# Kernel optimization log

Measured on AMD Instinct MI355X. Metric: run time of the kernel, lower is better.

The kernel has to match this reference:

```python
import jax, jax.numpy as jnp
import numpy as np

IOTA = 1.0 / 137.0
PHI = 0.618033988749894
N_SAMPLE = 5
N_SYM = 2048
HIDDEN = 2048
N_LIN_IN = 3
N_LIN_OUT = 9
EPS = 1e-9


def _instance_norm(x):
    # InstanceNorm1d, affine=False, unbatched (C, L): per-row mean/biased-var over last dim
    m = jnp.mean(x, axis=-1, keepdims=True)
    v = jnp.mean((x - m) ** 2, axis=-1, keepdims=True)
    return (x - m) * jax.lax.rsqrt(v + EPS)


def _lstm_cell(x, W_ih, W_hh, b_ih, b_hh):
    # torch.nn.LSTMCell with h0 = c0 = 0: the W_hh recurrent term is identically zero,
    # and f*c0 vanishes. Gate order (torch): i, f, g, o.
    gates = x @ W_ih.T + b_ih + b_hh  # [B, 4*HIDDEN]
    i, f, g, o = jnp.split(gates, 4, axis=-1)
    c = jax.nn.sigmoid(i) * jnp.tanh(g)
    return jax.nn.sigmoid(o) * jnp.tanh(c)


def setup_inputs() -> dict:
    key = jax.random.key(0)
    ks = jax.random.split(key, 10)
    s = 0.02
    return dict(
        signal=jax.random.normal(ks[0], (N_SAMPLE, N_SYM), jnp.float32),
        u1=jax.random.uniform(ks[1], (N_LIN_OUT, N_SYM), jnp.float32),
        u2=jax.random.uniform(ks[2], (N_LIN_OUT, HIDDEN), jnp.float32),
        bil_W=jax.random.normal(ks[3], (N_LIN_OUT, N_LIN_IN, N_LIN_IN), jnp.float32) * s,
        bil_b=jnp.zeros((N_LIN_OUT,), jnp.float32),
        Wih1=jax.random.normal(ks[4], (4 * HIDDEN, N_SYM), jnp.float32) * s,
        Whh1=jax.random.normal(ks[5], (4 * HIDDEN, HIDDEN), jnp.float32) * s,
        bih1=jnp.zeros((4 * HIDDEN,), jnp.float32),
        bhh1=jnp.zeros((4 * HIDDEN,), jnp.float32),
        Wih2=jax.random.normal(ks[6], (4 * HIDDEN, HIDDEN), jnp.float32) * s,
        Whh2=jax.random.normal(ks[7], (4 * HIDDEN, HIDDEN), jnp.float32) * s,
        bih2=jnp.zeros((4 * HIDDEN,), jnp.float32),
        bhh2=jnp.zeros((4 * HIDDEN,), jnp.float32),
        lin_W=jax.random.normal(ks[8], (N_SAMPLE * N_SYM, HIDDEN), jnp.float32) * s,
        lin_b=jnp.zeros((N_SAMPLE * N_SYM,), jnp.float32),
    )


def reference(signal, u1, u2, bil_W, bil_b, Wih1, Whh1, bih1, bhh1,
              Wih2, Whh2, bih2, bhh2, lin_W, lin_b):
    x = _instance_norm(signal.T)                    # [N_SYM, 5]
    fr = jnp.fft.rfft(x, axis=-1)                   # [N_SYM, 3] complex64
    b = jnp.nan_to_num(fr.real * fr.imag, nan=IOTA, posinf=1.0, neginf=IOTA)
    b = jax.nn.softmax(jax.nn.sigmoid(b), axis=1)   # [N_SYM, 3]
    # nn.Bilinear: out[n,k] = x1[n,i] W[k,i,j] x2[n,j] + b[k]
    b = jnp.einsum('ni,kij,nj->nk', b, bil_W, b) + bil_b  # [N_SYM, 9]
    b = IOTA + b.T * (u1 < PHI).astype(b.dtype)     # stochastic mask -> [9, N_SYM]
    h = _lstm_cell(b, Wih1, Whh1, bih1, bhh1)       # [9, HIDDEN]
    h = IOTA + h * (u2 < PHI).astype(h.dtype)
    h = _lstm_cell(h, Wih2, Whh2, bih2, bhh2)       # [9, HIDDEN]
    out = (h @ lin_W.T + lin_b).reshape(N_SAMPLE, N_SYM, N_LIN_OUT)  # view([5, N_SYM, 9])
    out = jax.nn.softmax(_instance_norm(out.sum(2)), axis=1)         # [5, N_SYM]
    return out
```

## Files before the change

### kernel.cpp

```cpp
#include <hip/hip_runtime.h>
#include <math.h>

#define IOTA_F (1.0f / 137.0f)
#define PHI_F  0.618033988749894f

__device__ __forceinline__ float sigm(float x) { return 1.0f / (1.0f + expf(-x)); }

__device__ __forceinline__ float nan2num(float v) {
    if (isnan(v)) return IOTA_F;
    if (isinf(v)) return v > 0.0f ? 1.0f : IOTA_F;
    return v;
}

__global__ void k_pre(const float* __restrict__ signal,
                      const float* __restrict__ u1,
                      const float* __restrict__ bilW,
                      const float* __restrict__ bilb,
                      float* __restrict__ B1)
{
    int s = blockIdx.x * blockDim.x + threadIdx.x;
    if (s >= 2048) return;

    float x0 = signal[0 * 2048 + s];
    float x1 = signal[1 * 2048 + s];
    float x2 = signal[2 * 2048 + s];
    float x3 = signal[3 * 2048 + s];
    float x4 = signal[4 * 2048 + s];

    float mean = (x0 + x1 + x2 + x3 + x4) * 0.2f;
    float d0 = x0 - mean, d1 = x1 - mean, d2 = x2 - mean, d3 = x3 - mean, d4 = x4 - mean;
    float var = (d0 * d0 + d1 * d1 + d2 * d2 + d3 * d3 + d4 * d4) * 0.2f;
    float r = 1.0f / sqrtf(var + 1e-9f);
    d0 *= r; d1 *= r; d2 *= r; d3 *= r; d4 *= r;

    const float c1 = 0.30901699437494742f;
    const float c2 = -0.80901699437494745f;
    const float s1 = 0.95105651629515357f;
    const float s2 = 0.58778525229247314f;

    float re1 = d0 + c1 * (d1 + d4) + c2 * (d2 + d3);
    float im1 = -(s1 * (d1 - d4) + s2 * (d2 - d3));
    float re2 = d0 + c2 * (d1 + d4) + c1 * (d2 + d3);
    float im2 = -s2 * (d1 - d4) + s1 * (d2 - d3);

    float p1 = nan2num(re1 * im1);
    float p2 = nan2num(re2 * im2);
    float g0 = 0.5f;
    float g1 = sigm(p1);
    float g2 = sigm(p2);

    float mx = fmaxf(g0, fmaxf(g1, g2));
    float e0 = expf(g0 - mx), e1 = expf(g1 - mx), e2 = expf(g2 - mx);
    float inv = 1.0f / (e0 + e1 + e2);
    float w[3] = { e0 * inv, e1 * inv, e2 * inv };

    #pragma unroll
    for (int kk = 0; kk < 9; ++kk) {
        float acc = bilb[kk];
        #pragma unroll
        for (int i = 0; i < 3; ++i)
            #pragma unroll
            for (int j = 0; j < 3; ++j)
                acc += w[i] * bilW[kk * 9 + i * 3 + j] * w[j];
        float mask = (u1[kk * 2048 + s] < PHI_F) ? 1.0f : 0.0f;
        B1[kk * 2048 + s] = IOTA_F + acc * mask;
    }
}

template <bool MASK>
__global__ __launch_bounds__(256) void k_lstm_fused(
    const float* __restrict__ Bv,
    const float* __restrict__ W,
    const float* __restrict__ b1,
    const float* __restrict__ b2,
    const float* __restrict__ u,
    float* __restrict__ Bout)
{
    __shared__ float lds[4][4][3][9];

    const int tid  = threadIdx.x;
    const int w    = tid >> 6;
    const int lane = tid & 63;
    const int grp  = lane >> 4;
    const int li   = lane & 15;

    const int q = blockIdx.x * 4 + grp;

    const float4* __restrict__ B4 = reinterpret_cast<const float4*>(Bv);
    const float4* __restrict__ Wi = reinterpret_cast<const float4*>(W) + (size_t)q * 512;
    const float4* __restrict__ Wg = Wi + (size_t)4096 * 512;
    const float4* __restrict__ Wo = Wi + (size_t)6144 * 512;

    float acc[3][9];
    #pragma unroll
    for (int r = 0; r < 3; ++r)
        #pragma unroll
        for (int m = 0; m < 9; ++m) acc[r][m] = 0.0f;

    const int kb4 = w * 128;

    #pragma unroll 2
    for (int it = 0; it < 8; ++it) {
        const int idx = kb4 + it * 16 + li;
        float4 bv[9];
        #pragma unroll
        for (int m = 0; m < 9; ++m) bv[m] = B4[m * 512 + idx];
        float4 wv0 = Wi[idx];
        float4 wv1 = Wg[idx];
        float4 wv2 = Wo[idx];
        #pragma unroll
        for (int m = 0; m < 9; ++m) {
            acc[0][m] = fmaf(wv0.x, bv[m].x, acc[0][m]);
            acc[0][m] = fmaf(wv0.y, bv[m].y, acc[0][m]);
            acc[0][m] = fmaf(wv0.z, bv[m].z, acc[0][m]);
            acc[0][m] = fmaf(wv0.w, bv[m].w, acc[0][m]);
            acc[1][m] = fmaf(wv1.x, bv[m].x, acc[1][m]);
            acc[1][m] = fmaf(wv1.y, bv[m].y, acc[1][m]);
            acc[1][m] = fmaf(wv1.z, bv[m].z, acc[1][m]);
            acc[1][m] = fmaf(wv1.w, bv[m].w, acc[1][m]);
            acc[2][m] = fmaf(wv2.x, bv[m].x, acc[2][m]);
            acc[2][m] = fmaf(wv2.y, bv[m].y, acc[2][m]);
            acc[2][m] = fmaf(wv2.z, bv[m].z, acc[2][m]);
            acc[2][m] = fmaf(wv2.w, bv[m].w, acc[2][m]);
        }
    }

    #pragma unroll
    for (int r = 0; r < 3; ++r)
        #pragma unroll
        for (int m = 0; m < 9; ++m) {
            float v = acc[r][m];
            v += __shfl_xor(v, 1);
            v += __shfl_xor(v, 2);
            v += __shfl_xor(v, 4);
            v += __shfl_xor(v, 8);
            acc[r][m] = v;
        }

    if (li == 0) {
        #pragma unroll
        for (int r = 0; r < 3; ++r)
            #pragma unroll
            for (int m = 0; m < 9; ++m)
                lds[w][grp][r][m] = acc[r][m];
    }
    __syncthreads();

    if (tid < 36) {
        const int qq = tid / 9;
        const int m  = tid - qq * 9;
        const int qg = blockIdx.x * 4 + qq;
        float iv = lds[0][qq][0][m] + lds[1][qq][0][m] + lds[2][qq][0][m] + lds[3][qq][0][m];
        float gv = lds[0][qq][1][m] + lds[1][qq][1][m] + lds[2][qq][1][m] + lds[3][qq][1][m];
        float ov = lds[0][qq][2][m] + lds[1][qq][2][m] + lds[2][qq][2][m] + lds[3][qq][2][m];
        iv += b1[qg] + b2[qg];
        gv += b1[4096 + qg] + b2[4096 + qg];
        ov += b1[6144 + qg] + b2[6144 + qg];
        float c = sigm(iv) * tanhf(gv);
        float h = sigm(ov) * tanhf(c);
        if (MASK) h = IOTA_F + h * ((u[m * 2048 + qg] < PHI_F) ? 1.0f : 0.0f);
        Bout[m * 2048 + qg] = h;
    }
}

template <int R>
__global__ __launch_bounds__(256) void k_gemvR(
    const float* __restrict__ Bv,
    const float* __restrict__ W,
    const float* __restrict__ bias,
    float* __restrict__ Out,
    int nrows)
{
    __shared__ float lds[4][4 * R][9];

    const int tid  = threadIdx.x;
    const int w    = tid >> 6;
    const int lane = tid & 63;
    const int grp  = lane >> 4;
    const int li   = lane & 15;

    const int rowB = blockIdx.x * 4 * R;
    const int row0 = rowB + grp * R;

    const float4* __restrict__ B4 = reinterpret_cast<const float4*>(Bv);
    const float4* __restrict__ W0 = reinterpret_cast<const float4*>(W) + (size_t)row0 * 512;

    float acc[R][9];
    #pragma unroll
    for (int r = 0; r < R; ++r)
        #pragma unroll
        for (int m = 0; m < 9; ++m) acc[r][m] = 0.0f;

    const int kb4 = w * 128;

    #pragma unroll 2
    for (int it = 0; it < 8; ++it) {
        const int idx = kb4 + it * 16 + li;
        float4 bv[9];
        #pragma unroll
        for (int m = 0; m < 9; ++m) bv[m] = B4[m * 512 + idx];
        #pragma unroll
        for (int r = 0; r < R; ++r) {
            float4 wv = W0[(size_t)r * 512 + idx];
            #pragma unroll
            for (int m = 0; m < 9; ++m) {
                acc[r][m] = fmaf(wv.x, bv[m].x, acc[r][m]);
                acc[r][m] = fmaf(wv.y, bv[m].y, acc[r][m]);
                acc[r][m] = fmaf(wv.z, bv[m].z, acc[r][m]);
                acc[r][m] = fmaf(wv.w, bv[m].w, acc[r][m]);
            }
        }
    }

    #pragma unroll
    for (int r = 0; r < R; ++r)
        #pragma unroll
        for (int m = 0; m < 9; ++m) {
            float v = acc[r][m];
            v += __shfl_xor(v, 1);
            v += __shfl_xor(v, 2);
            v += __shfl_xor(v, 4);
            v += __shfl_xor(v, 8);
            acc[r][m] = v;
        }

    if (li == 0) {
        #pragma unroll
        for (int r = 0; r < R; ++r)
            #pragma unroll
            for (int m = 0; m < 9; ++m)
                lds[w][grp * R + r][m] = acc[r][m];
    }
    __syncthreads();

    for (int t = tid; t < 4 * R * 9; t += 256) {
        const int row = t / 9;
        const int m   = t - row * 9;
        float v = lds[0][row][m] + lds[1][row][m] + lds[2][row][m] + lds[3][row][m];
        const int grow = rowB + row;
        Out[(size_t)m * nrows + grow] = v + bias[grow];
    }
}

__device__ __forceinline__ float block_reduce(float v, float* red, int tid, int op) {
    #pragma unroll
    for (int off = 32; off > 0; off >>= 1) {
        float o = __shfl_xor(v, off);
        v = op ? fmaxf(v, o) : (v + o);
    }
    __syncthreads();
    if ((tid & 63) == 0) red[tid >> 6] = v;
    __syncthreads();
    float r = red[0];
    #pragma unroll
    for (int w = 1; w < 8; ++w) r = op ? fmaxf(r, red[w]) : (r + red[w]);
    return r;
}

__global__ void k_final(const float* __restrict__ Z,
                        float* __restrict__ out)
{
    __shared__ float t[2048];
    __shared__ float red[8];
    const int a = blockIdx.x;
    const int tid = threadIdx.x;

    for (int s = tid; s < 2048; s += 512) {
        const float* zp = Z + a * 18432 + s * 9;
        float acc = 0.0f;
        #pragma unroll
        for (int k = 0; k < 9; ++k) acc += zp[k];
        t[s] = acc;
    }
    __syncthreads();

    float l0 = t[tid], l1 = t[tid + 512], l2 = t[tid + 1024], l3 = t[tid + 1536];

    float ssum = block_reduce(l0 + l1 + l2 + l3, red, tid, 0);
    float mean = ssum * (1.0f / 2048.0f);
    float e0 = l0 - mean, e1 = l1 - mean, e2 = l2 - mean, e3 = l3 - mean;
    float vsum = block_reduce(e0 * e0 + e1 * e1 + e2 * e2 + e3 * e3, red, tid, 0);
    float rstd = 1.0f / sqrtf(vsum * (1.0f / 2048.0f) + 1e-9f);
    float xn0 = e0 * rstd, xn1 = e1 * rstd, xn2 = e2 * rstd, xn3 = e3 * rstd;

    float mx = block_reduce(fmaxf(fmaxf(xn0, xn1), fmaxf(xn2, xn3)), red, tid, 1);
    float ex0 = expf(xn0 - mx), ex1 = expf(xn1 - mx), ex2 = expf(xn2 - mx), ex3 = expf(xn3 - mx);
    float esum = block_reduce(ex0 + ex1 + ex2 + ex3, red, tid, 0);
    float inv = 1.0f / esum;

    out[a * 2048 + tid]        = ex0 * inv;
    out[a * 2048 + tid + 512]  = ex1 * inv;
    out[a * 2048 + tid + 1024] = ex2 * inv;
    out[a * 2048 + tid + 1536] = ex3 * inv;
}

extern "C" void kernel_launch(void* const* d_in, const int* in_sizes, int n_in,
                              void* d_out, int out_size, void* d_ws, size_t ws_size,
                              hipStream_t stream)
{
    const float* signal = (const float*)d_in[0];
    const float* u1     = (const float*)d_in[1];
    const float* u2     = (const float*)d_in[2];
    const float* bilW   = (const float*)d_in[3];
    const float* bilb   = (const float*)d_in[4];
    const float* Wih1   = (const float*)d_in[5];
    const float* bih1   = (const float*)d_in[7];
    const float* bhh1   = (const float*)d_in[8];
    const float* Wih2   = (const float*)d_in[9];
    const float* bih2   = (const float*)d_in[11];
    const float* bhh2   = (const float*)d_in[12];
    const float* linW   = (const float*)d_in[13];
    const float* linb   = (const float*)d_in[14];

    float* out = (float*)d_out;
    float* ws  = (float*)d_ws;

    float* B1 = ws;
    float* B2 = ws + 18432;
    float* B3 = B1;
    float* Z  = ws + 36864;

    k_pre<<<8, 256, 0, stream>>>(signal, u1, bilW, bilb, B1);

    k_lstm_fused<true><<<512, 256, 0, stream>>>(B1, Wih1, bih1, bhh1, u2, B2);
    k_lstm_fused<false><<<512, 256, 0, stream>>>(B2, Wih2, bih2, bhh2, nullptr, B3);

    k_gemvR<5><<<512, 256, 0, stream>>>(B3, linW, linb, Z, 10240);

    k_final<<<5, 512, 0, stream>>>(Z, out);
}
```

Baseline: 56.06 us.

## Split K across 8 groups per row and prefetch weights into registers

The LSTM and final GEMV kernels now split the 2048-long reduction into 8 chunks spread over the sixteen 16-lane groups of each block. Each block handles 2 rows instead of 4, which doubles the grid to 1024 blocks. All weight float4s for a thread are loaded up front so more bytes are in flight per thread, and activations are loaded one m at a time. The aim is more memory-level parallelism and occupancy for these bandwidth-bound weight streams, at the cost of a wider cross-group LDS reduction and more blocks. The preprocessing kernel's launch shape changes from 8x256 to 32x64.

```diff
diff --git a/kernel.cpp b/kernel.cpp
--- a/kernel.cpp
+++ b/kernel.cpp
@@ -76,7 +76,7 @@
     const float* __restrict__ u,
     float* __restrict__ Bout)
 {
-    __shared__ float lds[4][4][3][9];
+    __shared__ float lds[2][8][3][9];
 
     const int tid  = threadIdx.x;
     const int w    = tid >> 6;
@@ -84,12 +84,24 @@
     const int grp  = lane >> 4;
     const int li   = lane & 15;
 
-    const int q = blockIdx.x * 4 + grp;
+    const int G  = w * 4 + grp;
+    const int qi = G >> 3;
+    const int kc = G & 7;
+    const int q  = blockIdx.x * 2 + qi;
 
     const float4* __restrict__ B4 = reinterpret_cast<const float4*>(Bv);
     const float4* __restrict__ Wi = reinterpret_cast<const float4*>(W) + (size_t)q * 512;
-    const float4* __restrict__ Wg = Wi + (size_t)4096 * 512;
-    const float4* __restrict__ Wo = Wi + (size_t)6144 * 512;
+
+    const int kb4 = kc * 64;
+
+    float4 wp[3][4];
+    #pragma unroll
+    for (int it = 0; it < 4; ++it) {
+        const int idx = kb4 + it * 16 + li;
+        wp[0][it] = Wi[idx];
+        wp[1][it] = Wi[(size_t)4096 * 512 + idx];
+        wp[2][it] = Wi[(size_t)6144 * 512 + idx];
+    }
 
     float acc[3][9];
     #pragma unroll
@@ -97,31 +109,19 @@
         #pragma unroll
         for (int m = 0; m < 9; ++m) acc[r][m] = 0.0f;
 
-    const int kb4 = w * 128;
-
-    #pragma unroll 2
-    for (int it = 0; it < 8; ++it) {
+    #pragma unroll
+    for (int it = 0; it < 4; ++it) {
         const int idx = kb4 + it * 16 + li;
-        float4 bv[9];
-        #pragma unroll
-        for (int m = 0; m < 9; ++m) bv[m] = B4[m * 512 + idx];
-        float4 wv0 = Wi[idx];
-        float4 wv1 = Wg[idx];
-        float4 wv2 = Wo[idx];
         #pragma unroll
         for (int m = 0; m < 9; ++m) {
-            acc[0][m] = fmaf(wv0.x, bv[m].x, acc[0][m]);
-            acc[0][m] = fmaf(wv0.y, bv[m].y, acc[0][m]);
-            acc[0][m] = fmaf(wv0.z, bv[m].z, acc[0][m]);
-            acc[0][m] = fmaf(wv0.w, bv[m].w, acc[0][m]);
-            acc[1][m] = fmaf(wv1.x, bv[m].x, acc[1][m]);
-            acc[1][m] = fmaf(wv1.y, bv[m].y, acc[1][m]);
-            acc[1][m] = fmaf(wv1.z, bv[m].z, acc[1][m]);
-            acc[1][m] = fmaf(wv1.w, bv[m].w, acc[1][m]);
-            acc[2][m] = fmaf(wv2.x, bv[m].x, acc[2][m]);
-            acc[2][m] = fmaf(wv2.y, bv[m].y, acc[2][m]);
-            acc[2][m] = fmaf(wv2.z, bv[m].z, acc[2][m]);
-            acc[2][m] = fmaf(wv2.w, bv[m].w, acc[2][m]);
+            float4 bv = B4[m * 512 + idx];
+            #pragma unroll
+            for (int r = 0; r < 3; ++r) {
+                acc[r][m] = fmaf(wp[r][it].x, bv.x, acc[r][m]);
+                acc[r][m] = fmaf(wp[r][it].y, bv.y, acc[r][m]);
+                acc[r][m] = fmaf(wp[r][it].z, bv.z, acc[r][m]);
+                acc[r][m] = fmaf(wp[r][it].w, bv.w, acc[r][m]);
+            }
         }
     }
 
@@ -142,17 +142,21 @@
         for (int r = 0; r < 3; ++r)
             #pragma unroll
             for (int m = 0; m < 9; ++m)
-                lds[w][grp][r][m] = acc[r][m];
-    }
-    __syncthreads();
-
-    if (tid < 36) {
+                lds[qi][kc][r][m] = acc[r][m];
+    }
+    __syncthreads();
+
+    if (tid < 18) {
         const int qq = tid / 9;
         const int m  = tid - qq * 9;
-        const int qg = blockIdx.x * 4 + qq;
-        float iv = lds[0][qq][0][m] + lds[1][qq][0][m] + lds[2][qq][0][m] + lds[3][qq][0][m];
-        float gv = lds[0][qq][1][m] + lds[1][qq][1][m] + lds[2][qq][1][m] + lds[3][qq][1][m];
-        float ov = lds[0][qq][2][m] + lds[1][qq][2][m] + lds[2][qq][2][m] + lds[3][qq][2][m];
+        const int qg = blockIdx.x * 2 + qq;
+        float iv = 0.0f, gv = 0.0f, ov = 0.0f;
+        #pragma unroll
+        for (int k = 0; k < 8; ++k) {
+            iv += lds[qq][k][0][m];
+            gv += lds[qq][k][1][m];
+            ov += lds[qq][k][2][m];
+        }
         iv += b1[qg] + b2[qg];
         gv += b1[4096 + qg] + b2[4096 + qg];
         ov += b1[6144 + qg] + b2[6144 + qg];
@@ -171,7 +175,7 @@
     float* __restrict__ Out,
     int nrows)
 {
-    __shared__ float lds[4][4 * R][9];
+    __shared__ float lds[2][8][R][9];
 
     const int tid  = threadIdx.x;
     const int w    = tid >> 6;
@@ -179,35 +183,47 @@
     const int grp  = lane >> 4;
     const int li   = lane & 15;
 
-    const int rowB = blockIdx.x * 4 * R;
-    const int row0 = rowB + grp * R;
+    const int G  = w * 4 + grp;
+    const int h  = G >> 3;
+    const int kc = G & 7;
+
+    const int rowB = blockIdx.x * 2 * R;
+    const int row0 = rowB + h * R;
 
     const float4* __restrict__ B4 = reinterpret_cast<const float4*>(Bv);
     const float4* __restrict__ W0 = reinterpret_cast<const float4*>(W) + (size_t)row0 * 512;
 
+    const int kb4 = kc * 64;
+
     float acc[R][9];
     #pragma unroll
     for (int r = 0; r < R; ++r)
         #pragma unroll
         for (int m = 0; m < 9; ++m) acc[r][m] = 0.0f;
 
-    const int kb4 = w * 128;
-
-    #pragma unroll 2
-    for (int it = 0; it < 8; ++it) {
-        const int idx = kb4 + it * 16 + li;
-        float4 bv[9];
-        #pragma unroll
-        for (int m = 0; m < 9; ++m) bv[m] = B4[m * 512 + idx];
-        #pragma unroll
-        for (int r = 0; r < R; ++r) {
-            float4 wv = W0[(size_t)r * 512 + idx];
+    #pragma unroll
+    for (int st = 0; st < 2; ++st) {
+        float4 wp[R][2];
+        #pragma unroll
+        for (int it = 0; it < 2; ++it) {
+            const int idx = kb4 + (st * 2 + it) * 16 + li;
+            #pragma unroll
+            for (int r = 0; r < R; ++r)
+                wp[r][it] = W0[(size_t)r * 512 + idx];
+        }
+        #pragma unroll
+        for (int it = 0; it < 2; ++it) {
+            const int idx = kb4 + (st * 2 + it) * 16 + li;
             #pragma unroll
             for (int m = 0; m < 9; ++m) {
-                acc[r][m] = fmaf(wv.x, bv[m].x, acc[r][m]);
-                acc[r][m] = fmaf(wv.y, bv[m].y, acc[r][m]);
-                acc[r][m] = fmaf(wv.z, bv[m].z, acc[r][m]);
-                acc[r][m] = fmaf(wv.w, bv[m].w, acc[r][m]);
+                float4 bv = B4[m * 512 + idx];
+                #pragma unroll
+                for (int r = 0; r < R; ++r) {
+                    acc[r][m] = fmaf(wp[r][it].x, bv.x, acc[r][m]);
+                    acc[r][m] = fmaf(wp[r][it].y, bv.y, acc[r][m]);
+                    acc[r][m] = fmaf(wp[r][it].z, bv.z, acc[r][m]);
+                    acc[r][m] = fmaf(wp[r][it].w, bv.w, acc[r][m]);
+                }
             }
         }
     }
@@ -229,14 +245,18 @@
         for (int r = 0; r < R; ++r)
             #pragma unroll
             for (int m = 0; m < 9; ++m)
-                lds[w][grp * R + r][m] = acc[r][m];
-    }
-    __syncthreads();
-
-    for (int t = tid; t < 4 * R * 9; t += 256) {
-        const int row = t / 9;
-        const int m   = t - row * 9;
-        float v = lds[0][row][m] + lds[1][row][m] + lds[2][row][m] + lds[3][row][m];
+                lds[h][kc][r][m] = acc[r][m];
+    }
+    __syncthreads();
+
+    if (tid < 2 * R * 9) {
+        const int row = tid / 9;
+        const int m   = tid - row * 9;
+        const int hh  = row / R;
+        const int rr  = row - hh * R;
+        float v = 0.0f;
+        #pragma unroll
+        for (int k = 0; k < 8; ++k) v += lds[hh][k][rr][m];
         const int grow = rowB + row;
         Out[(size_t)m * nrows + grow] = v + bias[grow];
     }
@@ -320,12 +340,12 @@
     float* B3 = B1;
     float* Z  = ws + 36864;
 
-    k_pre<<<8, 256, 0, stream>>>(signal, u1, bilW, bilb, B1);
-
-    k_lstm_fused<true><<<512, 256, 0, stream>>>(B1, Wih1, bih1, bhh1, u2, B2);
-    k_lstm_fused<false><<<512, 256, 0, stream>>>(B2, Wih2, bih2, bhh2, nullptr, B3);
-
-    k_gemvR<5><<<512, 256, 0, stream>>>(B3, linW, linb, Z, 10240);
+    k_pre<<<32, 64, 0, stream>>>(signal, u1, bilW, bilb, B1);
+
+    k_lstm_fused<true><<<1024, 256, 0, stream>>>(B1, Wih1, bih1, bhh1, u2, B2);
+    k_lstm_fused<false><<<1024, 256, 0, stream>>>(B2, Wih2, bih2, bhh2, nullptr, B3);
+
+    k_gemvR<5><<<1024, 256, 0, stream>>>(B3, linW, linb, Z, 10240);
 
     k_final<<<5, 512, 0, stream>>>(Z, out);
 }
```

Measured after the change: 61.95 us. 1.1x slower.

## Fuse preprocessing into first LSTM kernel and final softmax into last GEMV

Applied to the files above, without the earlier changes.

Each block of the first LSTM kernel now recomputes the full normalization/FFT/bilinear preprocessing into shared memory, removing the separate pre kernel. The final instance-norm/softmax is folded into the output GEMV using an atomic counter so the last finishing block performs it. This removes two kernel launches and a global round trip, at the cost of redundant per-block preprocessing work, large LDS usage limiting occupancy, and a serialized single-block tail.

```diff
diff --git a/kernel.cpp b/kernel.cpp
--- a/kernel.cpp
+++ b/kernel.cpp
@@ -3,6 +3,7 @@
 
 #define IOTA_F (1.0f / 137.0f)
 #define PHI_F  0.618033988749894f
+#define NBLK   512
 
 __device__ __forceinline__ float sigm(float x) { return 1.0f / (1.0f + expf(-x)); }
 
@@ -12,68 +13,167 @@
     return v;
 }
 
-__global__ void k_pre(const float* __restrict__ signal,
-                      const float* __restrict__ u1,
-                      const float* __restrict__ bilW,
-                      const float* __restrict__ bilb,
-                      float* __restrict__ B1)
-{
-    int s = blockIdx.x * blockDim.x + threadIdx.x;
-    if (s >= 2048) return;
-
-    float x0 = signal[0 * 2048 + s];
-    float x1 = signal[1 * 2048 + s];
-    float x2 = signal[2 * 2048 + s];
-    float x3 = signal[3 * 2048 + s];
-    float x4 = signal[4 * 2048 + s];
-
-    float mean = (x0 + x1 + x2 + x3 + x4) * 0.2f;
-    float d0 = x0 - mean, d1 = x1 - mean, d2 = x2 - mean, d3 = x3 - mean, d4 = x4 - mean;
-    float var = (d0 * d0 + d1 * d1 + d2 * d2 + d3 * d3 + d4 * d4) * 0.2f;
-    float r = 1.0f / sqrtf(var + 1e-9f);
-    d0 *= r; d1 *= r; d2 *= r; d3 *= r; d4 *= r;
-
-    const float c1 = 0.30901699437494742f;
-    const float c2 = -0.80901699437494745f;
-    const float s1 = 0.95105651629515357f;
-    const float s2 = 0.58778525229247314f;
-
-    float re1 = d0 + c1 * (d1 + d4) + c2 * (d2 + d3);
-    float im1 = -(s1 * (d1 - d4) + s2 * (d2 - d3));
-    float re2 = d0 + c2 * (d1 + d4) + c1 * (d2 + d3);
-    float im2 = -s2 * (d1 - d4) + s1 * (d2 - d3);
-
-    float p1 = nan2num(re1 * im1);
-    float p2 = nan2num(re2 * im2);
-    float g0 = 0.5f;
-    float g1 = sigm(p1);
-    float g2 = sigm(p2);
-
-    float mx = fmaxf(g0, fmaxf(g1, g2));
-    float e0 = expf(g0 - mx), e1 = expf(g1 - mx), e2 = expf(g2 - mx);
-    float inv = 1.0f / (e0 + e1 + e2);
-    float w[3] = { e0 * inv, e1 * inv, e2 * inv };
-
-    #pragma unroll
-    for (int kk = 0; kk < 9; ++kk) {
-        float acc = bilb[kk];
-        #pragma unroll
-        for (int i = 0; i < 3; ++i)
+__device__ void pre_into_lds(int tid,
+                             const float* __restrict__ signal,
+                             const float* __restrict__ u1,
+                             const float* __restrict__ bilW,
+                             const float* __restrict__ bilb,
+                             float* __restrict__ Bsf)
+{
+    #pragma unroll
+    for (int k = 0; k < 8; ++k) {
+        const int s = k * 256 + tid;
+
+        float x0 = signal[0 * 2048 + s];
+        float x1 = signal[1 * 2048 + s];
+        float x2 = signal[2 * 2048 + s];
+        float x3 = signal[3 * 2048 + s];
+        float x4 = signal[4 * 2048 + s];
+
+        float mean = (x0 + x1 + x2 + x3 + x4) * 0.2f;
+        float d0 = x0 - mean, d1 = x1 - mean, d2 = x2 - mean, d3 = x3 - mean, d4 = x4 - mean;
+        float var = (d0 * d0 + d1 * d1 + d2 * d2 + d3 * d3 + d4 * d4) * 0.2f;
+        float r = 1.0f / sqrtf(var + 1e-9f);
+        d0 *= r; d1 *= r; d2 *= r; d3 *= r; d4 *= r;
+
+        const float c1 = 0.30901699437494742f;
+        const float c2 = -0.80901699437494745f;
+        const float s1 = 0.95105651629515357f;
+        const float s2 = 0.58778525229247314f;
+
+        float re1 = d0 + c1 * (d1 + d4) + c2 * (d2 + d3);
+        float im1 = -(s1 * (d1 - d4) + s2 * (d2 - d3));
+        float re2 = d0 + c2 * (d1 + d4) + c1 * (d2 + d3);
+        float im2 = -s2 * (d1 - d4) + s1 * (d2 - d3);
+
+        float p1 = nan2num(re1 * im1);
+        float p2 = nan2num(re2 * im2);
+        float g0 = 0.5f;
+        float g1 = sigm(p1);
+        float g2 = sigm(p2);
+
+        float mx = fmaxf(g0, fmaxf(g1, g2));
+        float e0 = expf(g0 - mx), e1 = expf(g1 - mx), e2 = expf(g2 - mx);
+        float inv = 1.0f / (e0 + e1 + e2);
+        float w[3] = { e0 * inv, e1 * inv, e2 * inv };
+
+        #pragma unroll
+        for (int kk = 0; kk < 9; ++kk) {
+            float acc = bilb[kk];
             #pragma unroll
-            for (int j = 0; j < 3; ++j)
-                acc += w[i] * bilW[kk * 9 + i * 3 + j] * w[j];
-        float mask = (u1[kk * 2048 + s] < PHI_F) ? 1.0f : 0.0f;
-        B1[kk * 2048 + s] = IOTA_F + acc * mask;
-    }
-}
-
-template <bool MASK>
-__global__ __launch_bounds__(256) void k_lstm_fused(
+            for (int i = 0; i < 3; ++i)
+                #pragma unroll
+                for (int j = 0; j < 3; ++j)
+                    acc += w[i] * bilW[kk * 9 + i * 3 + j] * w[j];
+            float mask = (u1[kk * 2048 + s] < PHI_F) ? 1.0f : 0.0f;
+            Bsf[kk * 2048 + s] = IOTA_F + acc * mask;
+        }
+    }
+}
+
+__global__ __launch_bounds__(256, 2) void k_pre_lstm1(
+    const float* __restrict__ signal, const float* __restrict__ u1,
+    const float* __restrict__ bilW, const float* __restrict__ bilb,
+    const float* __restrict__ W,
+    const float* __restrict__ b1,
+    const float* __restrict__ b2,
+    const float* __restrict__ u,
+    float* __restrict__ Bout)
+{
+    __shared__ float Bsf[9 * 2048];
+    __shared__ float red[4][4][3][9];
+
+    const int tid  = threadIdx.x;
+    const int w    = tid >> 6;
+    const int lane = tid & 63;
+    const int grp  = lane >> 4;
+    const int li   = lane & 15;
+
+    pre_into_lds(tid, signal, u1, bilW, bilb, Bsf);
+    __syncthreads();
+
+    const float4* __restrict__ Bs4 = reinterpret_cast<const float4*>(Bsf);
+    const int q = blockIdx.x * 4 + grp;
+
+    const float4* __restrict__ Wi = reinterpret_cast<const float4*>(W) + (size_t)q * 512;
+    const float4* __restrict__ Wg = Wi + (size_t)4096 * 512;
+    const float4* __restrict__ Wo = Wi + (size_t)6144 * 512;
+
+    float acc[3][9];
+    #pragma unroll
+    for (int r = 0; r < 3; ++r)
+        #pragma unroll
+        for (int m = 0; m < 9; ++m) acc[r][m] = 0.0f;
+
+    const int kb4 = w * 128;
+
+    #pragma unroll 2
+    for (int it = 0; it < 8; ++it) {
+        const int idx = kb4 + it * 16 + li;
+        float4 wv0 = Wi[idx];
+        float4 wv1 = Wg[idx];
+        float4 wv2 = Wo[idx];
+        #pragma unroll
+        for (int m = 0; m < 9; ++m) {
+            float4 bv = Bs4[m * 512 + idx];
+            acc[0][m] = fmaf(wv0.x, bv.x, acc[0][m]);
+            acc[0][m] = fmaf(wv0.y, bv.y, acc[0][m]);
+            acc[0][m] = fmaf(wv0.z, bv.z, acc[0][m]);
+            acc[0][m] = fmaf(wv0.w, bv.w, acc[0][m]);
+            acc[1][m] = fmaf(wv1.x, bv.x, acc[1][m]);
+            acc[1][m] = fmaf(wv1.y, bv.y, acc[1][m]);
+            acc[1][m] = fmaf(wv1.z, bv.z, acc[1][m]);
+            acc[1][m] = fmaf(wv1.w, bv.w, acc[1][m]);
+            acc[2][m] = fmaf(wv2.x, bv.x, acc[2][m]);
+            acc[2][m] = fmaf(wv2.y, bv.y, acc[2][m]);
+            acc[2][m] = fmaf(wv2.z, bv.z, acc[2][m]);
+            acc[2][m] = fmaf(wv2.w, bv.w, acc[2][m]);
+        }
+    }
+
+    #pragma unroll
+    for (int r = 0; r < 3; ++r)
+        #pragma unroll
+        for (int m = 0; m < 9; ++m) {
+            float v = acc[r][m];
+            v += __shfl_xor(v, 1);
+            v += __shfl_xor(v, 2);
+            v += __shfl_xor(v, 4);
+            v += __shfl_xor(v, 8);
+            acc[r][m] = v;
+        }
+
+    if (li == 0) {
+        #pragma unroll
+        for (int r = 0; r < 3; ++r)
+            #pragma unroll
+            for (int m = 0; m < 9; ++m)
+                red[w][grp][r][m] = acc[r][m];
+    }
+    __syncthreads();
+
+    if (tid < 36) {
+        const int qq = tid / 9;
+        const int m  = tid - qq * 9;
+        const int qg = blockIdx.x * 4 + qq;
+        float iv = red[0][qq][0][m] + red[1][qq][0][m] + red[2][qq][0][m] + red[3][qq][0][m];
+        float gv = red[0][qq][1][m] + red[1][qq][1][m] + red[2][qq][1][m] + red[3][qq][1][m];
+        float ov = red[0][qq][2][m] + red[1][qq][2][m] + red[2][qq][2][m] + red[3][qq][2][m];
+        iv += b1[qg] + b2[qg];
+        gv += b1[4096 + qg] + b2[4096 + qg];
+        ov += b1[6144 + qg] + b2[6144 + qg];
+        float c = sigm(iv) * tanhf(gv);
+        float h = sigm(ov) * tanhf(c);
+        h = IOTA_F + h * ((u[m * 2048 + qg] < PHI_F) ? 1.0f : 0.0f);
+        Bout[m * 2048 + qg] = h;
+    }
+}
+
+__global__ __launch_bounds__(256, 2) void k_lstm2(
     const float* __restrict__ Bv,
     const float* __restrict__ W,
     const float* __restrict__ b1,
     const float* __restrict__ b2,
-    const float* __restrict__ u,
     float* __restrict__ Bout)
 {
     __shared__ float lds[4][4][3][9];
@@ -158,20 +258,79 @@
         ov += b1[6144 + qg] + b2[6144 + qg];
         float c = sigm(iv) * tanhf(gv);
         float h = sigm(ov) * tanhf(c);
-        if (MASK) h = IOTA_F + h * ((u[m * 2048 + qg] < PHI_F) ? 1.0f : 0.0f);
         Bout[m * 2048 + qg] = h;
     }
 }
 
+__device__ __forceinline__ float block_reduce256(float v, float* red, int tid, int op) {
+    #pragma unroll
+    for (int off = 32; off > 0; off >>= 1) {
+        float o = __shfl_xor(v, off);
+        v = op ? fmaxf(v, o) : (v + o);
+    }
+    __syncthreads();
+    if ((tid & 63) == 0) red[tid >> 6] = v;
+    __syncthreads();
+    float r = op ? fmaxf(fmaxf(red[0], red[1]), fmaxf(red[2], red[3]))
+                 : (red[0] + red[1] + red[2] + red[3]);
+    return r;
+}
+
+__device__ void final_phase(int a, int tid, float* __restrict__ t, float* __restrict__ red,
+                            const float* __restrict__ Z, float* __restrict__ out)
+{
+    for (int s = tid; s < 2048; s += 256) {
+        const float* zp = Z + a * 18432 + s * 9;
+        float acc = 0.0f;
+        #pragma unroll
+        for (int k = 0; k < 9; ++k) acc += zp[k];
+        t[s] = acc;
+    }
+    __syncthreads();
+
+    float l[8];
+    #pragma unroll
+    for (int j = 0; j < 8; ++j) l[j] = t[tid + j * 256];
+
+    float lsum = 0.0f;
+    #pragma unroll
+    for (int j = 0; j < 8; ++j) lsum += l[j];
+    float ssum = block_reduce256(lsum, red, tid, 0);
+    float mean = ssum * (1.0f / 2048.0f);
+
+    float vs = 0.0f;
+    #pragma unroll
+    for (int j = 0; j < 8; ++j) { l[j] -= mean; vs += l[j] * l[j]; }
+    float vsum = block_reduce256(vs, red, tid, 0);
+    float rstd = 1.0f / sqrtf(vsum * (1.0f / 2048.0f) + 1e-9f);
+
+    float lmx = -1e30f;
+    #pragma unroll
+    for (int j = 0; j < 8; ++j) { l[j] *= rstd; lmx = fmaxf(lmx, l[j]); }
+    float mx = block_reduce256(lmx, red, tid, 1);
+
+    float es = 0.0f;
+    #pragma unroll
+    for (int j = 0; j < 8; ++j) { l[j] = expf(l[j] - mx); es += l[j]; }
+    float esum = block_reduce256(es, red, tid, 0);
+    float inv = 1.0f / esum;
+
+    #pragma unroll
+    for (int j = 0; j < 8; ++j)
+        out[a * 2048 + tid + j * 256] = l[j] * inv;
+}
+
 template <int R>
-__global__ __launch_bounds__(256) void k_gemvR(
+__global__ __launch_bounds__(256, 2) void k_gemvR_final(
     const float* __restrict__ Bv,
     const float* __restrict__ W,
     const float* __restrict__ bias,
-    float* __restrict__ Out,
-    int nrows)
-{
-    __shared__ float lds[4][4 * R][9];
+    float* __restrict__ Z,
+    float* __restrict__ out,
+    int* __restrict__ counter)
+{
+    __shared__ float arena[2052];
+    __shared__ int   is_last;
 
     const int tid  = threadIdx.x;
     const int w    = tid >> 6;
@@ -229,69 +388,35 @@
         for (int r = 0; r < R; ++r)
             #pragma unroll
             for (int m = 0; m < 9; ++m)
-                lds[w][grp * R + r][m] = acc[r][m];
+                arena[(w * 4 * R + grp * R + r) * 9 + m] = acc[r][m];
     }
     __syncthreads();
 
     for (int t = tid; t < 4 * R * 9; t += 256) {
         const int row = t / 9;
         const int m   = t - row * 9;
-        float v = lds[0][row][m] + lds[1][row][m] + lds[2][row][m] + lds[3][row][m];
+        float v = arena[(0 * 4 * R + row) * 9 + m] + arena[(1 * 4 * R + row) * 9 + m]
+                + arena[(2 * 4 * R + row) * 9 + m] + arena[(3 * 4 * R + row) * 9 + m];
         const int grow = rowB + row;
-        Out[(size_t)m * nrows + grow] = v + bias[grow];
-    }
-}
-
-__device__ __forceinline__ float block_reduce(float v, float* red, int tid, int op) {
-    #pragma unroll
-    for (int off = 32; off > 0; off >>= 1) {
-        float o = __shfl_xor(v, off);
-        v = op ? fmaxf(v, o) : (v + o);
-    }
-    __syncthreads();
-    if ((tid & 63) == 0) red[tid >> 6] = v;
-    __syncthreads();
-    float r = red[0];
-    #pragma unroll
-    for (int w = 1; w < 8; ++w) r = op ? fmaxf(r, red[w]) : (r + red[w]);
-    return r;
-}
-
-__global__ void k_final(const float* __restrict__ Z,
-                        float* __restrict__ out)
-{
-    __shared__ float t[2048];
-    __shared__ float red[8];
-    const int a = blockIdx.x;
-    const int tid = threadIdx.x;
-
-    for (int s = tid; s < 2048; s += 512) {
-        const float* zp = Z + a * 18432 + s * 9;
-        float acc = 0.0f;
-        #pragma unroll
-        for (int k = 0; k < 9; ++k) acc += zp[k];
-        t[s] = acc;
-    }
-    __syncthreads();
-
-    float l0 = t[tid], l1 = t[tid + 512], l2 = t[tid + 1024], l3 = t[tid + 1536];
-
-    float ssum = block_reduce(l0 + l1 + l2 + l3, red, tid, 0);
-    float mean = ssum * (1.0f / 2048.0f);
-    float e0 = l0 - mean, e1 = l1 - mean, e2 = l2 - mean, e3 = l3 - mean;
-    float vsum = block_reduce(e0 * e0 + e1 * e1 + e2 * e2 + e3 * e3, red, tid, 0);
-    float rstd = 1.0f / sqrtf(vsum * (1.0f / 2048.0f) + 1e-9f);
-    float xn0 = e0 * rstd, xn1 = e1 * rstd, xn2 = e2 * rstd, xn3 = e3 * rstd;
-
-    float mx = block_reduce(fmaxf(fmaxf(xn0, xn1), fmaxf(xn2, xn3)), red, tid, 1);
-    float ex0 = expf(xn0 - mx), ex1 = expf(xn1 - mx), ex2 = expf(xn2 - mx), ex3 = expf(xn3 - mx);
-    float esum = block_reduce(ex0 + ex1 + ex2 + ex3, red, tid, 0);
-    float inv = 1.0f / esum;
-
-    out[a * 2048 + tid]        = ex0 * inv;
-    out[a * 2048 + tid + 512]  = ex1 * inv;
-    out[a * 2048 + tid + 1024] = ex2 * inv;
-    out[a * 2048 + tid + 1536] = ex3 * inv;
+        Z[(size_t)m * 10240 + grow] = v + bias[grow];
+    }
+
+    __syncthreads();
+    __threadfence();
+    if (tid == 0) {
+        int old = __hip_atomic_fetch_add(counter, 1, __ATOMIC_ACQ_REL,
+                                         __HIP_MEMORY_SCOPE_AGENT);
+        is_last = (old == NBLK - 1);
+    }
+    __syncthreads();
+    if (!is_last) return;
+
+    __threadfence();
+    __syncthreads();
+    for (int a = 0; a < 5; ++a) {
+        final_phase(a, tid, arena, arena + 2048, Z, out);
+        __syncthreads();
+    }
 }
 
 extern "C" void kernel_launch(void* const* d_in, const int* in_sizes, int n_in,
@@ -315,17 +440,17 @@
     float* out = (float*)d_out;
     float* ws  = (float*)d_ws;
 
-    float* B1 = ws;
-    float* B2 = ws + 18432;
-    float* B3 = B1;
-    float* Z  = ws + 36864;
-
-    k_pre<<<8, 256, 0, stream>>>(signal, u1, bilW, bilb, B1);
-
-    k_lstm_fused<true><<<512, 256, 0, stream>>>(B1, Wih1, bih1, bhh1, u2, B2);
-    k_lstm_fused<false><<<512, 256, 0, stream>>>(B2, Wih2, bih2, bhh2, nullptr, B3);
-
-    k_gemvR<5><<<512, 256, 0, stream>>>(B3, linW, linb, Z, 10240);
-
-    k_final<<<5, 512, 0, stream>>>(Z, out);
-}
+    float* B2      = ws;
+    float* B3      = ws + 18432;
+    float* Z       = ws + 36864;
+    int*   counter = (int*)(ws + 36864 + 92160);
+
+    hipMemsetAsync(counter, 0, sizeof(int), stream);
+
+    k_pre_lstm1<<<NBLK, 256, 0, stream>>>(signal, u1, bilW, bilb,
+                                          Wih1, bih1, bhh1, u2, B2);
+
+    k_lstm2<<<NBLK, 256, 0, stream>>>(B2, Wih2, bih2, bhh2, B3);
+
+    k_gemvR_final<5><<<NBLK, 256, 0, stream>>>(B3, linW, linb, Z, out, counter);
+}
```

Result: slower. 134.1 us (+139.2%).
